# Kernel tuning notes

Hardware: AMD Instinct MI355X
Metric: run time of the kernel (lower is better)

## Reference

```python
import jax, jax.numpy as jnp
import numpy as np

K = 2048  # num_embeddings
D = 64    # embedding_dim


def setup_inputs() -> dict:
    key = jax.random.key(0)
    k1, k2 = jax.random.split(key)
    inputs = jax.random.normal(k1, (64, 32, 32, D), dtype=jnp.float32)
    # tf.random_uniform_initializer default: U[0, 1)
    embeddings = jax.random.uniform(k2, (K, D), dtype=jnp.float32)
    return {"inputs": inputs, "embeddings": embeddings}


def reference(inputs, embeddings):
    input_shape = inputs.shape
    flat_inputs = inputs.reshape(-1, D)  # [N, D]
    distances = (
        jnp.sum(flat_inputs ** 2, axis=1, keepdims=True)
        - 2.0 * jnp.matmul(flat_inputs, embeddings.T)
        + jnp.sum(embeddings ** 2, axis=1)
    )
    encoding_indices = jnp.argmin(distances, axis=1)  # [N]
    quantized = embeddings[encoding_indices].reshape(input_shape)
    # straight-through estimator
    quantized = inputs + jax.lax.stop_gradient(quantized - inputs)
    return quantized, encoding_indices, flat_inputs
```

## Files before the change

### kernel.cpp

```cpp
#include <hip/hip_runtime.h>
#include <cfloat>

#define N_TOTAL 65536
#define DIM     64
#define NEMB    2048

typedef __attribute__((ext_vector_type(8))) _Float16 half8;
typedef __attribute__((ext_vector_type(4))) float    floatx4;

__global__ void prep_kernel(const float* __restrict__ emb,
                            half8* __restrict__ ehp, float* __restrict__ en) {
    const int t = blockIdx.x * 256 + threadIdx.x;
    {
        const int l   = t & 63;
        const int ks  = (t >> 6) & 1;
        const int g   = t >> 7;
        const int col = g * 16 + (l & 15);
        const int kb  = ks * 32 + (l >> 4) * 8;
        const float* s = emb + col * DIM + kb;
        float4 v0 = *(const float4*)s, v1 = *(const float4*)(s + 4);
        half8 hv;
        hv[0] = (_Float16)v0.x; hv[1] = (_Float16)v0.y;
        hv[2] = (_Float16)v0.z; hv[3] = (_Float16)v0.w;
        hv[4] = (_Float16)v1.x; hv[5] = (_Float16)v1.y;
        hv[6] = (_Float16)v1.z; hv[7] = (_Float16)v1.w;
        ehp[t] = hv;
    }
    if (t < NEMB * 4) {
        const int row = t >> 2, seg = t & 3;
        const float* s = emb + row * DIM + seg * 16;
        float acc = 0.f;
#pragma unroll
        for (int i = 0; i < 4; ++i) {
            float4 v = ((const float4*)s)[i];
            acc = fmaf(v.x, v.x, acc); acc = fmaf(v.y, v.y, acc);
            acc = fmaf(v.z, v.z, acc); acc = fmaf(v.w, v.w, acc);
        }
        acc += __shfl_xor(acc, 1, 64);
        acc += __shfl_xor(acc, 2, 64);
        if (seg == 0) en[row] = acc;
    }
}

__global__ __launch_bounds__(256, 4) void vq_mfma_kernel(
        const float* __restrict__ x, const float* __restrict__ emb,
        const uint4* __restrict__ ehp, const float* __restrict__ eng,
        float* __restrict__ quant, float* __restrict__ idxf,
        float* __restrict__ flat) {

    __shared__ uint4 Stage[4][512];
    __shared__ uint4 Mrg[2][64];

    const int t    = threadIdx.x;
    const int wave = t >> 6, lane = t & 63;
    const int n = lane & 15, q = lane >> 4;
    const int h = wave & 1, p = wave >> 1;
    const int blk0 = blockIdx.x * 64;
    const int row0 = blk0 + p * 32;

    {
        const float4* s4 = (const float4*)(x + (size_t)blk0 * DIM);
        float4*       d4 = (float4*)(flat + (size_t)blk0 * DIM);
#pragma unroll
        for (int i = 0; i < 4; ++i) d4[i * 256 + t] = s4[i * 256 + t];
    }

    half8 ah[2][2], al[2][2];
#pragma unroll
    for (int tl = 0; tl < 2; ++tl)
#pragma unroll
        for (int ks = 0; ks < 2; ++ks) {
            const float* pp = x + (size_t)(row0 + tl * 16 + n) * DIM + ks * 32 + q * 8;
            float4 v0 = *(const float4*)pp, v1 = *(const float4*)(pp + 4);
            float xv[8] = {v0.x, v0.y, v0.z, v0.w, v1.x, v1.y, v1.z, v1.w};
#pragma unroll
            for (int j = 0; j < 8; ++j) {
                _Float16 hh = (_Float16)xv[j];
                ah[tl][ks][j] = hh;
                al[tl][ks][j] = (_Float16)(xv[j] - (float)hh);
            }
        }

    unsigned best[8], sec[8];
#pragma unroll
    for (int r = 0; r < 8; ++r) { best[r] = 0u; sec[r] = 0u; }

    const char* ehb = (const char*)ehp;
    for (int st = 0; st < 16; ++st) {
        const int colbase = h * 1024 + st * 64;
        const int g0 = colbase >> 4;
        asm volatile("s_waitcnt lgkmcnt(0)" ::: "memory");
#pragma unroll
        for (int i = 0; i < 8; ++i) {
            const unsigned* gp =
                (const unsigned*)(ehb + (size_t)g0 * 2048 + i * 1024 + lane * 16);
            __builtin_amdgcn_global_load_lds(
                (const __attribute__((address_space(1))) unsigned*)gp,
                (__attribute__((address_space(3))) unsigned*)&Stage[wave][i * 64],
                16, 0, 0);
        }
        float en4[4];
#pragma unroll
        for (int s = 0; s < 4; ++s) en4[s] = eng[colbase + s * 16 + n];
        asm volatile("s_waitcnt vmcnt(0)" ::: "memory");

#pragma unroll
        for (int sub = 0; sub < 4; ++sub) {
            const float enh = fmaf(-0.5f, en4[sub], 128.0f);
            floatx4 a0 = {enh, enh, enh, enh};
            floatx4 a1 = a0;
#pragma unroll
            for (int ks = 0; ks < 2; ++ks) {
                half8 b = *(const half8*)&Stage[wave][(sub * 2 + ks) * 64 + lane];
                a0 = __builtin_amdgcn_mfma_f32_16x16x32_f16(ah[0][ks], b, a0, 0, 0, 0);
                a0 = __builtin_amdgcn_mfma_f32_16x16x32_f16(al[0][ks], b, a0, 0, 0, 0);
                a1 = __builtin_amdgcn_mfma_f32_16x16x32_f16(ah[1][ks], b, a1, 0, 0, 0);
                a1 = __builtin_amdgcn_mfma_f32_16x16x32_f16(al[1][ks], b, a1, 0, 0, 0);
            }
            const unsigned Lp = (unsigned)(63 - (st * 4 + sub));
#pragma unroll
            for (int r = 0; r < 8; ++r) {
                float v = (r < 4) ? a0[r] : a1[r - 4];
                unsigned key = (__float_as_uint(v) & 0xFFFFFFC0u) | Lp;
                unsigned lo  = best[r] < key ? best[r] : key;
                best[r] = best[r] > key ? best[r] : key;
                sec[r]  = sec[r] > lo ? sec[r] : lo;
            }
        }
    }

    unsigned bval[8], bcol[8], sval[8], scol[8];
#pragma unroll
    for (int r = 0; r < 8; ++r) {
        bval[r] = best[r] & 0xFFFFFFC0u;
        bcol[r] = (unsigned)(h * 1024 + (63 - (int)(best[r] & 63u)) * 16 + n);
        sval[r] = sec[r] & 0xFFFFFFC0u;
        scol[r] = (unsigned)(h * 1024 + (63 - (int)(sec[r] & 63u)) * 16 + n);
    }
#pragma unroll
    for (int m = 1; m < 16; m <<= 1) {
#pragma unroll
        for (int r = 0; r < 8; ++r) {
            unsigned ov  = (unsigned)__shfl_xor((int)bval[r], m, 64);
            unsigned oc  = (unsigned)__shfl_xor((int)bcol[r], m, 64);
            unsigned ov2 = (unsigned)__shfl_xor((int)sval[r], m, 64);
            unsigned oc2 = (unsigned)__shfl_xor((int)scol[r], m, 64);
            bool ow = (ov > bval[r]) || (ov == bval[r] && oc < bcol[r]);
            unsigned nbv = ow ? ov : bval[r], nbc = ow ? oc : bcol[r];
            unsigned lv  = ow ? bval[r] : ov, lc  = ow ? bcol[r] : oc;
            bool sv2 = (ov2 > sval[r]) || (ov2 == sval[r] && oc2 < scol[r]);
            unsigned bsv = sv2 ? ov2 : sval[r], bsc = sv2 ? oc2 : scol[r];
            bool s3 = (lv > bsv) || (lv == bsv && lc < bsc);
            sval[r] = s3 ? lv : bsv; scol[r] = s3 ? lc : bsc;
            bval[r] = nbv; bcol[r] = nbc;
        }
    }
    if (n == 0) {
#pragma unroll
        for (int r = 0; r < 8; ++r) {
            const int lr = p * 32 + (r >> 2) * 16 + q * 4 + (r & 3);
            Mrg[h][lr] = make_uint4(bval[r], bcol[r], sval[r], scol[r]);
        }
    }
    __syncthreads();

#pragma unroll
    for (int r = 0; r < 4; ++r) {
        const int lr   = wave * 16 + q * 4 + r;
        const int grow = blk0 + lr;
        uint4 c0v = Mrg[0][lr], c1v = Mrg[1][lr];
        int cand[4] = {(int)c0v.y, (int)c0v.w, (int)c1v.y, (int)c1v.w};
        float4 xv = *(const float4*)(x + (size_t)grow * DIM + n * 4);
        float pbest = -FLT_MAX; int cbest = 0;
        float4 ebest = {0.f, 0.f, 0.f, 0.f};
#pragma unroll
        for (int c = 0; c < 4; ++c) {
            float4 e = *(const float4*)(emb + (size_t)cand[c] * DIM + n * 4);
            float pp = (xv.x - 0.5f * e.x) * e.x + (xv.y - 0.5f * e.y) * e.y
                     + (xv.z - 0.5f * e.z) * e.z + (xv.w - 0.5f * e.w) * e.w;
#pragma unroll
            for (int m2 = 1; m2 < 16; m2 <<= 1) pp += __shfl_xor(pp, m2, 64);
            bool take = (pp > pbest) || (pp == pbest && cand[c] < cbest);
            pbest = take ? pp : pbest;
            cbest = take ? cand[c] : cbest;
            ebest.x = take ? e.x : ebest.x; ebest.y = take ? e.y : ebest.y;
            ebest.z = take ? e.z : ebest.z; ebest.w = take ? e.w : ebest.w;
        }
        *(float4*)(quant + (size_t)grow * DIM + n * 4) = ebest;
        if (n == 0) idxf[grow] = (float)cbest;
    }
}

extern "C" void kernel_launch(void* const* d_in, const int* in_sizes, int n_in,
                              void* d_out, int out_size, void* d_ws, size_t ws_size,
                              hipStream_t stream) {
    const float* x   = (const float*)d_in[0];
    const float* emb = (const float*)d_in[1];
    float* out   = (float*)d_out;
    float* quant = out;
    float* idxf  = out + (size_t)N_TOTAL * DIM;
    float* flat  = idxf + N_TOTAL;

    half8* ehp = (half8*)d_ws;
    float* en  = (float*)((char*)d_ws + (size_t)NEMB * DIM * 2);

    prep_kernel<<<64, 256, 0, stream>>>(emb, ehp, en);
    vq_mfma_kernel<<<N_TOTAL / 64, 256, 0, stream>>>(x, emb, (const uint4*)ehp, en,
                                                     quant, idxf, flat);
}
```

Baseline: 127.1 us.

## Double-buffer codebook staging in LDS and cache embedding norms in shared memory

Each wave's codebook staging is split into two 4KB buffers: the next tile is prefetched with global_load_lds while MFMAs run on the current one, replacing the old load-all-then-wait per 64-column step. The embedding norms are copied into shared memory once per block instead of read from global each step. B fragments are read with inline ds_read_b128. The extra LDS (8KB norms) and the lower launch bound of 3 may reduce occupancy in exchange for overlapping load latency.

```diff
diff --git a/kernel.cpp b/kernel.cpp
--- a/kernel.cpp
+++ b/kernel.cpp
@@ -42,13 +42,14 @@
     }
 }
 
-__global__ __launch_bounds__(256, 4) void vq_mfma_kernel(
+__global__ __launch_bounds__(256, 3) void vq_mfma_kernel(
         const float* __restrict__ x, const float* __restrict__ emb,
-        const uint4* __restrict__ ehp, const float* __restrict__ eng,
+        const char* __restrict__ ehb, const float* __restrict__ eng,
         float* __restrict__ quant, float* __restrict__ idxf,
         float* __restrict__ flat) {
 
-    __shared__ uint4 Stage[4][512];
+    __shared__ uint4 Stage[4][2][256];
+    __shared__ float EnS[NEMB];
     __shared__ uint4 Mrg[2][64];
 
     const int t    = threadIdx.x;
@@ -64,6 +65,12 @@
 #pragma unroll
         for (int i = 0; i < 4; ++i) d4[i * 256 + t] = s4[i * 256 + t];
     }
+    {
+        const float4* s4 = (const float4*)eng;
+        float4*       d4 = (float4*)EnS;
+#pragma unroll
+        for (int i = 0; i < 2; ++i) d4[i * 256 + t] = s4[i * 256 + t];
+    }
 
     half8 ah[2][2], al[2][2];
 #pragma unroll
@@ -81,43 +88,70 @@
             }
         }
 
+    __syncthreads();
+
     unsigned best[8], sec[8];
 #pragma unroll
     for (int r = 0; r < 8; ++r) { best[r] = 0u; sec[r] = 0u; }
 
-    const char* ehb = (const char*)ehp;
-    for (int st = 0; st < 16; ++st) {
-        const int colbase = h * 1024 + st * 64;
-        const int g0 = colbase >> 4;
-        asm volatile("s_waitcnt lgkmcnt(0)" ::: "memory");
-#pragma unroll
-        for (int i = 0; i < 8; ++i) {
-            const unsigned* gp =
-                (const unsigned*)(ehb + (size_t)g0 * 2048 + i * 1024 + lane * 16);
-            __builtin_amdgcn_global_load_lds(
-                (const __attribute__((address_space(1))) unsigned*)gp,
-                (__attribute__((address_space(3))) unsigned*)&Stage[wave][i * 64],
-                16, 0, 0);
-        }
-        float en4[4];
-#pragma unroll
-        for (int s = 0; s < 4; ++s) en4[s] = eng[colbase + s * 16 + n];
-        asm volatile("s_waitcnt vmcnt(0)" ::: "memory");
-
-#pragma unroll
-        for (int sub = 0; sub < 4; ++sub) {
-            const float enh = fmaf(-0.5f, en4[sub], 128.0f);
+    const char* ebase = ehb + (size_t)h * 131072 + (size_t)lane * 16;
+
+#pragma unroll
+    for (int i = 0; i < 4; ++i)
+        __builtin_amdgcn_global_load_lds(
+            (const __attribute__((address_space(1))) unsigned*)(ebase + i * 1024),
+            (__attribute__((address_space(3))) unsigned*)&Stage[wave][0][i * 64],
+            16, 0, 0);
+
+#pragma unroll 2
+    for (int tile = 0; tile < 32; ++tile) {
+        const int buf = tile & 1;
+        if (tile < 31) {
+            asm volatile("s_waitcnt lgkmcnt(0)" ::: "memory");
+            const char* src = ebase + (size_t)(tile + 1) * 4096;
+#pragma unroll
+            for (int i = 0; i < 4; ++i)
+                __builtin_amdgcn_global_load_lds(
+                    (const __attribute__((address_space(1))) unsigned*)(src + i * 1024),
+                    (__attribute__((address_space(3))) unsigned*)&Stage[wave][buf ^ 1][i * 64],
+                    16, 0, 0);
+            asm volatile("s_waitcnt vmcnt(4)" ::: "memory");
+        } else {
+            asm volatile("s_waitcnt vmcnt(0)" ::: "memory");
+        }
+
+        half8 b00, b01, b10, b11;
+        {
+            const __attribute__((address_space(3))) char* sb =
+                (const __attribute__((address_space(3))) char*)&Stage[wave][buf][0];
+            asm volatile("ds_read_b128 %0, %4\n\t"
+                         "ds_read_b128 %1, %4 offset:1024\n\t"
+                         "ds_read_b128 %2, %4 offset:2048\n\t"
+                         "ds_read_b128 %3, %4 offset:3072\n\t"
+                         "s_waitcnt lgkmcnt(0)"
+                         : "=&v"(b00), "=&v"(b01), "=&v"(b10), "=&v"(b11)
+                         : "v"(sb + lane * 16));
+        }
+
+#pragma unroll
+        for (int sub = 0; sub < 2; ++sub) {
+            const int L = tile * 2 + sub;
+            const float env = EnS[h * 1024 + L * 16 + n];
+            const float enh = fmaf(-0.5f, env, 128.0f);
             floatx4 a0 = {enh, enh, enh, enh};
             floatx4 a1 = a0;
-#pragma unroll
-            for (int ks = 0; ks < 2; ++ks) {
-                half8 b = *(const half8*)&Stage[wave][(sub * 2 + ks) * 64 + lane];
-                a0 = __builtin_amdgcn_mfma_f32_16x16x32_f16(ah[0][ks], b, a0, 0, 0, 0);
-                a0 = __builtin_amdgcn_mfma_f32_16x16x32_f16(al[0][ks], b, a0, 0, 0, 0);
-                a1 = __builtin_amdgcn_mfma_f32_16x16x32_f16(ah[1][ks], b, a1, 0, 0, 0);
-                a1 = __builtin_amdgcn_mfma_f32_16x16x32_f16(al[1][ks], b, a1, 0, 0, 0);
-            }
-            const unsigned Lp = (unsigned)(63 - (st * 4 + sub));
+            half8 bk0 = sub ? b10 : b00;
+            half8 bk1 = sub ? b11 : b01;
+            a0 = __builtin_amdgcn_mfma_f32_16x16x32_f16(ah[0][0], bk0, a0, 0, 0, 0);
+            a0 = __builtin_amdgcn_mfma_f32_16x16x32_f16(al[0][0], bk0, a0, 0, 0, 0);
+            a1 = __builtin_amdgcn_mfma_f32_16x16x32_f16(ah[1][0], bk0, a1, 0, 0, 0);
+            a1 = __builtin_amdgcn_mfma_f32_16x16x32_f16(al[1][0], bk0, a1, 0, 0, 0);
+            a0 = __builtin_amdgcn_mfma_f32_16x16x32_f16(ah[0][1], bk1, a0, 0, 0, 0);
+            a0 = __builtin_amdgcn_mfma_f32_16x16x32_f16(al[0][1], bk1, a0, 0, 0, 0);
+            a1 = __builtin_amdgcn_mfma_f32_16x16x32_f16(ah[1][1], bk1, a1, 0, 0, 0);
+            a1 = __builtin_amdgcn_mfma_f32_16x16x32_f16(al[1][1], bk1, a1, 0, 0, 0);
+
+            const unsigned Lp = (unsigned)(63 - L);
 #pragma unroll
             for (int r = 0; r < 8; ++r) {
                 float v = (r < 4) ? a0[r] : a1[r - 4];
@@ -205,6 +239,6 @@
     float* en  = (float*)((char*)d_ws + (size_t)NEMB * DIM * 2);
 
     prep_kernel<<<64, 256, 0, stream>>>(emb, ehp, en);
-    vq_mfma_kernel<<<N_TOTAL / 64, 256, 0, stream>>>(x, emb, (const uint4*)ehp, en,
+    vq_mfma_kernel<<<N_TOTAL / 64, 256, 0, stream>>>(x, emb, (const char*)ehp, en,
                                                      quant, idxf, flat);
 }
```

Result: no change. 128.3 us (+1.0%).
